# Optimization experiments

Hardware: AMD Instinct MI355X
Metric: run time of the kernel (lower is better)

## Reference

```python
import jax, jax.numpy as jnp
import numpy as np

EPS_BN = 1e-5
CLAMP_MAX = 1e-10  # nn.Hardtanh(min_val=0, max_val=1e-10) on squared dists


def _three_nn(xyz1, xyz2):
    # xyz1: (b, n, 3), xyz2: (b, m, 3) -> sq dists (b, n, 3), idx (b, n, 3)
    d2 = (jnp.sum(xyz1 ** 2, -1, keepdims=True)
          - 2.0 * jnp.einsum('bnc,bmc->bnm', xyz1, xyz2)
          + jnp.sum(xyz2 ** 2, -1)[:, None, :])  # (b, n, m)
    neg, idx = jax.lax.top_k(-d2, 3)
    return -neg, idx


def _conv_bn_relu(x, W, b, g, beta):
    # x: (b, n, cin); 1x1 Conv2d == pointwise linear, BN over (batch, spatial)
    y = jnp.einsum('bnc,oc->bno', x, W) + b
    mean = jnp.mean(y, axis=(0, 1))
    var = jnp.mean((y - mean) ** 2, axis=(0, 1))
    y = (y - mean) * jax.lax.rsqrt(var + EPS_BN) * g + beta
    return jax.nn.relu(y)


def setup_inputs() -> dict:
    key = jax.random.key(0)
    ks = jax.random.split(key, 8)
    b, n, m, c1, c2 = 16, 4096, 1024, 256, 512
    mlp, dimin = [256, 256], [c1 + c2, 256]
    inp = {
        'xyz1': jax.random.normal(ks[0], (b, n, 3), jnp.float32),
        'xyz2': jax.random.normal(ks[1], (b, m, 3), jnp.float32),
        'points1': jax.random.normal(ks[2], (b, n, c1), jnp.float32),
        'points2': jax.random.normal(ks[3], (b, m, c2), jnp.float32),
        'W1': jax.random.normal(ks[4], (mlp[0], dimin[0]), jnp.float32) * 0.02,
        'b1': jnp.zeros((mlp[0],), jnp.float32),
        'g1': jnp.ones((mlp[0],), jnp.float32),
        'beta1': jnp.zeros((mlp[0],), jnp.float32),
        'W2': jax.random.normal(ks[5], (mlp[1], dimin[1]), jnp.float32) * 0.02,
        'b2': jnp.zeros((mlp[1],), jnp.float32),
        'g2': jnp.ones((mlp[1],), jnp.float32),
        'beta2': jnp.zeros((mlp[1],), jnp.float32),
    }
    return inp


def reference(xyz1, xyz2, points1, points2, W1, b1, g1, beta1, W2, b2, g2, beta2):
    dist, idx = _three_nn(xyz1, xyz2)                     # (b, n, 3)
    dist = jnp.clip(dist, 0.0, CLAMP_MAX)                 # Hardtanh(0, 1e-10)
    inv = 1.0 / dist
    weight = inv / jnp.sum(inv, axis=2, keepdims=True)    # (b, n, 3)
    neigh = jax.vmap(lambda p, i: p[i])(points2, idx)     # (b, n, 3, c2)
    interp = jnp.einsum('bnk,bnkc->bnc', weight, neigh)   # (b, n, c2)
    feat = jnp.concatenate([interp, points1], axis=2)     # (b, n, c2+c1)
    feat = _conv_bn_relu(feat, W1, b1, g1, beta1)
    feat = _conv_bn_relu(feat, W2, b2, g2, beta2)
    return jnp.transpose(feat, (0, 2, 1))                 # (b, c_out, n)
```

## Files before the change

### kernel.cpp

```cpp
#include <hip/hip_runtime.h>

typedef unsigned short u16;
typedef short sh8 __attribute__((ext_vector_type(8)));
typedef float floatx4 __attribute__((ext_vector_type(4)));
typedef float float4v __attribute__((ext_vector_type(4)));
typedef u16 us8 __attribute__((ext_vector_type(8)));
typedef u16 us4 __attribute__((ext_vector_type(4)));

#define NB    16
#define NPTS  4096
#define MPTS  1024
#define CC1   256
#define CC2   512
#define KK1   768
#define CCO   256
#define MT    (NB*NPTS)
#define MZ    (NB*MPTS)

__device__ __forceinline__ float b2f(u16 u) {
    union { unsigned i; float f; } v; v.i = ((unsigned)u) << 16; return v.f;
}
__device__ __forceinline__ u16 f2b(float f) {
    union { float f; unsigned i; } v; v.f = f;
    unsigned u = v.i;
    unsigned r = (u + 0x7fffu + ((u >> 16) & 1u)) >> 16;
    return (u16)r;
}
__device__ __forceinline__ float ldv(const void* p, size_t i, int f32) {
    return f32 ? ((const float*)p)[i] : b2f(((const u16*)p)[i]);
}
__device__ __forceinline__ void stv(void* p, size_t i, int f32, float v) {
    if (f32) ((float*)p)[i] = v; else ((u16*)p)[i] = f2b(v);
}
__device__ __forceinline__ void gl_lds16(const void* g, void* l) {
    __builtin_amdgcn_global_load_lds(
        (const __attribute__((address_space(1))) void*)g,
        (__attribute__((address_space(3))) void*)l, 16, 0, 0);
}

__global__ __launch_bounds__(256) void Pointnet_fp_module_33071248179394_kernel(
        const unsigned* g1bits, int* flag, float* stats,
        const void* W1, const void* W2, u16* Wa, u16* Wbp, u16* W2b) {
    const int f32 = (g1bits[0] == 0x3F800000u) ? 1 : 0;
    const int i = blockIdx.x * 256 + threadIdx.x;
    if (blockIdx.x == 0) {
        for (int k = threadIdx.x; k < 1024; k += 256) stats[k] = 0.f;
        if (threadIdx.x == 0) flag[0] = f32;
    }
    if (i < CCO * CC2) {
        int r = i >> 9, c = i & 511;
        Wa[i] = f2b(ldv(W1, (size_t)r * KK1 + c, f32));
    } else if (i < CCO * CC2 + CCO * CC1) {
        int k = i - CCO * CC2;
        int r = k >> 8, c = k & 255;
        Wbp[k] = f2b(ldv(W1, (size_t)r * KK1 + CC2 + c, f32));
    } else {
        int k = i - CCO * CC2 - CCO * CC1;
        W2b[k] = f2b(ldv(W2, k, f32));
    }
}

__global__ __launch_bounds__(512) void three_nn_k(
        const int* flagp, const void* xyz1, const void* xyz2,
        int* nidx, float* nw) {
    __shared__ float4 P[MPTS];
    __shared__ float md[512][3];
    __shared__ int   mi[512][3];
    const int f32 = flagp[0];
    const int bi = blockIdx.x >> 6;
    const int chunk = blockIdx.x & 63;
    const int t = threadIdx.x;
    const int ql = t & 63, sp = t >> 6;

    for (int p = t; p < MPTS; p += 512) {
        size_t s = (size_t)(bi * MPTS + p) * 3;
        P[p] = make_float4(ldv(xyz2, s, f32), ldv(xyz2, s + 1, f32),
                           ldv(xyz2, s + 2, f32), 0.f);
    }
    __syncthreads();

    const int q = chunk * 64 + ql;
    size_t s1 = (size_t)(bi * NPTS + q) * 3;
    const float qx = ldv(xyz1, s1 + 0, f32);
    const float qy = ldv(xyz1, s1 + 1, f32);
    const float qz = ldv(xyz1, s1 + 2, f32);

    float d0 = 3e38f, d1 = 3e38f, dv2 = 3e38f;
    int i0 = -1, i1 = -1, i2 = -1;
    const int jbeg = sp * 128, jend = jbeg + 128;
    #pragma unroll 4
    for (int j = jbeg; j < jend; j++) {
        float4 p = P[j];
        float dx = qx - p.x;
        float dy = qy - p.y;
        float dz = qz - p.z;
        float dd = fmaf(dx, dx, fmaf(dy, dy, dz * dz));
        if (dd < dv2) {
            if (dd < d0)      { dv2 = d1; i2 = i1; d1 = d0; i1 = i0; d0 = dd; i0 = j; }
            else if (dd < d1) { dv2 = d1; i2 = i1; d1 = dd; i1 = j; }
            else              { dv2 = dd; i2 = j; }
        }
    }
    md[t][0] = d0;  md[t][1] = d1;  md[t][2] = dv2;
    mi[t][0] = i0;  mi[t][1] = i1;  mi[t][2] = i2;
    __syncthreads();

    if (t < 64) {
        float b0 = 3e38f, b1 = 3e38f, b2v = 3e38f;
        int j0 = -1, j1 = -1, j2 = -1;
        #pragma unroll
        for (int s = 0; s < 8; s++) {
            int base = s * 64 + t;
            #pragma unroll
            for (int k = 0; k < 3; k++) {
                float d = md[base][k];
                int ji = mi[base][k];
                if (d < b0)      { b2v = b1; j2 = j1; b1 = b0; j1 = j0; b0 = d; j0 = ji; }
                else if (d < b1) { b2v = b1; j2 = j1; b1 = d; j1 = ji; }
                else if (d < b2v){ b2v = d; j2 = ji; }
            }
        }
        float e0 = fminf(fmaxf(b0, 0.f), 1e-10f);
        float e1 = fminf(fmaxf(b1, 0.f), 1e-10f);
        float e2 = fminf(fmaxf(b2v, 0.f), 1e-10f);
        float v0 = 1.0f / e0, v1 = 1.0f / e1, v2 = 1.0f / e2;
        float s = v0 + v1 + v2;
        const size_t gq = ((size_t)bi * NPTS + chunk * 64 + t) * 3;
        nidx[gq + 0] = j0; nidx[gq + 1] = j1; nidx[gq + 2] = j2;
        nw[gq + 0] = v0 / s; nw[gq + 1] = v1 / s; nw[gq + 2] = v2 / s;
    }
}

template<int K, int NW>
__global__ __launch_bounds__(128 * NW, 2) void gemm_z_k(
        const int* flagp, const void* __restrict__ A, const u16* __restrict__ B,
        u16* __restrict__ Y) {
    constexpr int T  = 128 * NW;
    constexpr int NT = NW * 64;
    __shared__ u16 As[128 * 32];
    __shared__ u16 Bs[NT * 32];
    const int f32 = flagp[0];
    const int tid = threadIdx.x;
    const int m0 = blockIdx.x * 128;
    const int n0 = blockIdx.y * NT;
    const int wave = tid >> 6, lane = tid & 63;
    const int wm = wave & 1, wn = wave >> 1;
    const int l16 = lane & 15, quad = lane >> 4;

    floatx4 acc[4][4];
    #pragma unroll
    for (int i = 0; i < 4; i++)
        #pragma unroll
        for (int j = 0; j < 4; j++)
            acc[i][j] = (floatx4){0.f, 0.f, 0.f, 0.f};

    for (int kb = 0; kb < K; kb += 32) {
        __syncthreads();
        #pragma unroll
        for (int c = tid; c < 512; c += T) {
            int row = c >> 2, c4 = c & 3;
            if (f32) {
                const float* ap = (const float*)A + (size_t)(m0 + row) * K + kb + c4 * 8;
                float4v a = *(const float4v*)ap;
                float4v b = *(const float4v*)(ap + 4);
                us8 o;
                #pragma unroll
                for (int k = 0; k < 4; k++) { o[k] = f2b(a[k]); o[k + 4] = f2b(b[k]); }
                *(us8*)(As + c * 8) = o;
            } else {
                gl_lds16((const u16*)A + (size_t)(m0 + row) * K + kb + c4 * 8,
                         As + c * 8);
            }
        }
        #pragma unroll
        for (int c = tid; c < NT * 4; c += T) {
            int row = c >> 2, c4 = c & 3;
            gl_lds16(B + (size_t)(n0 + row) * K + kb + c4 * 8, Bs + c * 8);
        }
        __syncthreads();

        sh8 af[4], bfr[4];
        #pragma unroll
        for (int i = 0; i < 4; i++)
            af[i] = *(const sh8*)(As + (wm * 64 + i * 16 + l16) * 32 + quad * 8);
        #pragma unroll
        for (int j = 0; j < 4; j++)
            bfr[j] = *(const sh8*)(Bs + (wn * 64 + j * 16 + l16) * 32 + quad * 8);
        #pragma unroll
        for (int i = 0; i < 4; i++)
            #pragma unroll
            for (int j = 0; j < 4; j++)
                acc[i][j] = __builtin_amdgcn_mfma_f32_16x16x32_bf16(
                                bfr[j], af[i], acc[i][j], 0, 0, 0);
    }

    #pragma unroll
    for (int i = 0; i < 4; i++) {
        int row = m0 + wm * 64 + i * 16 + l16;
        #pragma unroll
        for (int j = 0; j < 4; j++) {
            int colb = wn * 64 + j * 16 + quad * 4;
            us4 o;
            #pragma unroll
            for (int r = 0; r < 4; r++)
                o[r] = f2b(acc[i][j][r]);
            *(us4*)(Y + (size_t)row * CCO + n0 + colb) = o;
        }
    }
}

template<bool GATHER, bool BN1>
__global__ __launch_bounds__(256, 4) void gemm_mt_k(
        const int* flagp, const void* __restrict__ Asrc,
        const u16* __restrict__ B, const void* __restrict__ bias,
        const int* __restrict__ nidx, const float* __restrict__ nw,
        const u16* __restrict__ Zb,
        u16* __restrict__ Y, float* __restrict__ sum, float* __restrict__ sq,
        const float* __restrict__ nsum, const float* __restrict__ nsq,
        const void* __restrict__ ng, const void* __restrict__ nbeta) {
    __shared__ u16 As[64 * 256];
    __shared__ float sSum[256], sSq[256];
    __shared__ int   sIdx[GATHER ? 192 : 1];
    __shared__ float sW[GATHER ? 192 : 1];
    __shared__ float ssc[BN1 ? 256 : 1], ssh[BN1 ? 256 : 1];
    const int f32 = flagp[0];
    const int tid = threadIdx.x;
    const int m0 = blockIdx.x * 64;
    const int wn = tid >> 6, lane = tid & 63;
    const int l16 = lane & 15, quad = lane >> 4;

    sSum[tid] = 0.f; sSq[tid] = 0.f;
    if (BN1) {
        const float invM = 1.0f / (float)MT;
        float mean = nsum[tid] * invM;
        float var = nsq[tid] * invM - mean * mean;
        float sc = rsqrtf(var + 1e-5f) * ldv(ng, tid, f32);
        ssc[tid] = sc;
        ssh[tid] = ldv(nbeta, tid, f32) - mean * sc;
    }
    if (GATHER && tid < 64) {
        size_t q3 = (size_t)(m0 + tid) * 3;
        #pragma unroll
        for (int k = 0; k < 3; k++) {
            sIdx[tid * 3 + k] = nidx[q3 + k];
            sW[tid * 3 + k]   = nw[q3 + k];
        }
    }
    if (BN1) __syncthreads();

    #pragma unroll
    for (int c = tid; c < 2048; c += 256) {
        int r = c >> 5, cp = c & 31;
        int col = ((cp ^ (r & 7)) << 3);
        if (BN1) {
            us8 a = *(const us8*)((const u16*)Asrc + (size_t)(m0 + r) * 256 + col);
            us8 o;
            #pragma unroll
            for (int k = 0; k < 8; k++)
                o[k] = f2b(fmaxf(b2f((u16)a[k]) * ssc[col + k] + ssh[col + k], 0.f));
            *(us8*)(As + c * 8) = o;
        } else if (f32) {
            const float* ap = (const float*)Asrc + (size_t)(m0 + r) * 256 + col;
            float4v a = *(const float4v*)ap;
            float4v b = *(const float4v*)(ap + 4);
            us8 o;
            #pragma unroll
            for (int k = 0; k < 4; k++) { o[k] = f2b(a[k]); o[k + 4] = f2b(b[k]); }
            *(us8*)(As + c * 8) = o;
        } else {
            gl_lds16((const u16*)Asrc + (size_t)(m0 + r) * 256 + col, As + c * 8);
        }
    }
    __syncthreads();

    floatx4 acc[4][4];
    #pragma unroll
    for (int i = 0; i < 4; i++)
        #pragma unroll
        for (int j = 0; j < 4; j++)
            acc[i][j] = (floatx4){0.f, 0.f, 0.f, 0.f};

    #pragma unroll 2
    for (int kb = 0; kb < 256; kb += 32) {
        sh8 af[4], bfr[4];
        #pragma unroll
        for (int j = 0; j < 4; j++)
            bfr[j] = *(const sh8*)(B + (size_t)(wn * 64 + j * 16 + l16) * 256
                                     + kb + quad * 8);
        #pragma unroll
        for (int i = 0; i < 4; i++) {
            int r = i * 16 + l16;
            int cp = ((kb >> 3) + quad) ^ (l16 & 7);
            af[i] = *(const sh8*)(As + r * 256 + (cp << 3));
        }
        #pragma unroll
        for (int i = 0; i < 4; i++)
            #pragma unroll
            for (int j = 0; j < 4; j++)
                acc[i][j] = __builtin_amdgcn_mfma_f32_16x16x32_bf16(
                                bfr[j], af[i], acc[i][j], 0, 0, 0);
    }

    float bvv[4][4];
    #pragma unroll
    for (int j = 0; j < 4; j++)
        #pragma unroll
        for (int r = 0; r < 4; r++)
            bvv[j][r] = ldv(bias, wn * 64 + j * 16 + quad * 4 + r, f32);

    float cs[4][4], css[4][4];
    #pragma unroll
    for (int j = 0; j < 4; j++)
        #pragma unroll
        for (int r = 0; r < 4; r++) { cs[j][r] = 0.f; css[j][r] = 0.f; }

    const int zbase = GATHER ? ((m0 >> 12) << 10) : 0;
    #pragma unroll
    for (int i = 0; i < 4; i++) {
        int rl = i * 16 + l16;
        const u16 *z0 = nullptr, *z1 = nullptr, *z2 = nullptr;
        float w0 = 0.f, w1 = 0.f, w2 = 0.f;
        if (GATHER) {
            int i0 = sIdx[rl * 3 + 0], i1 = sIdx[rl * 3 + 1], i2 = sIdx[rl * 3 + 2];
            w0 = sW[rl * 3 + 0]; w1 = sW[rl * 3 + 1]; w2 = sW[rl * 3 + 2];
            z0 = Zb + (size_t)(zbase + i0) * CCO;
            z1 = Zb + (size_t)(zbase + i1) * CCO;
            z2 = Zb + (size_t)(zbase + i2) * CCO;
        }
        u16* yrow = Y + (size_t)(m0 + rl) * CCO;
        #pragma unroll
        for (int j = 0; j < 4; j++) {
            int colb = wn * 64 + j * 16 + quad * 4;
            us4 o;
            if (GATHER) {
                us4 zv0 = *(const us4*)(z0 + colb);
                us4 zv1 = *(const us4*)(z1 + colb);
                us4 zv2 = *(const us4*)(z2 + colb);
                #pragma unroll
                for (int r = 0; r < 4; r++) {
                    float v = acc[i][j][r] + bvv[j][r]
                            + w0 * b2f((u16)zv0[r]) + w1 * b2f((u16)zv1[r])
                            + w2 * b2f((u16)zv2[r]);
                    cs[j][r] += v; css[j][r] += v * v;
                    o[r] = f2b(v);
                }
            } else {
                #pragma unroll
                for (int r = 0; r < 4; r++) {
                    float v = acc[i][j][r] + bvv[j][r];
                    cs[j][r] += v; css[j][r] += v * v;
                    o[r] = f2b(v);
                }
            }
            *(us4*)(yrow + colb) = o;
        }
    }
    #pragma unroll
    for (int j = 0; j < 4; j++)
        #pragma unroll
        for (int r = 0; r < 4; r++) {
            float a = cs[j][r], b = css[j][r];
            #pragma unroll
            for (int m = 1; m < 16; m <<= 1) {
                a += __shfl_xor(a, m, 64);
                b += __shfl_xor(b, m, 64);
            }
            if (l16 == 0) {
                int cl = wn * 64 + j * 16 + quad * 4 + r;
                atomicAdd(&sSum[cl], a);
                atomicAdd(&sSq[cl], b);
            }
        }
    __syncthreads();
    atomicAdd(&sum[tid], sSum[tid]);
    atomicAdd(&sq[tid], sSq[tid]);
}

__global__ void bn_out_k(const int* flagp, const u16* Y, void* Out,
                         const float* sum, const float* sq,
                         const void* g, const void* beta) {
    __shared__ float tile[64][65];
    const int f32 = flagp[0];
    const int bi = blockIdx.z;
    const int p0 = blockIdx.x * 64;
    const int c0 = blockIdx.y * 64;
    const int t = threadIdx.x;
    const int cr = t & 63, rq = t >> 6;
    const float invM = 1.0f / (float)MT;

    const int c = c0 + cr;
    float mean = sum[c] * invM;
    float var = sq[c] * invM - mean * mean;
    float sc = rsqrtf(var + 1e-5f) * ldv(g, c, f32);
    float sh = ldv(beta, c, f32) - mean * sc;

    for (int r = rq; r < 64; r += 4) {
        int m = bi * NPTS + p0 + r;
        float v = b2f(Y[(size_t)m * CCO + c]) * sc + sh;
        tile[r][cr] = fmaxf(v, 0.f);
    }
    __syncthreads();
    for (int r = rq; r < 64; r += 4) {
        size_t o = ((size_t)bi * CCO + (c0 + r)) * NPTS + p0 + cr;
        stv(Out, o, f32, tile[cr][r]);
    }
}

extern "C" void kernel_launch(void* const* d_in, const int* in_sizes, int n_in,
                              void* d_out, int out_size, void* d_ws, size_t ws_size,
                              hipStream_t stream) {
    const void* xyz1    = d_in[0];
    const void* xyz2    = d_in[1];
    const void* points1 = d_in[2];
    const void* points2 = d_in[3];
    const void* W1      = d_in[4];
    const void* b1      = d_in[5];
    const void* g1      = d_in[6];
    const void* be1     = d_in[7];
    const void* W2      = d_in[8];
    const void* b2      = d_in[9];
    const void* g2      = d_in[10];
    const void* be2     = d_in[11];
    char* ws = (char*)d_ws;

    int*   flag  = (int*)(ws + 0);
    float* sum1  = (float*)(ws + 4096);
    float* sq1   = (float*)(ws + 5120);
    float* sum2  = (float*)(ws + 6144);
    float* sq2   = (float*)(ws + 7168);
    int*   nidx  = (int*)(ws + 20480);
    float* nw    = (float*)(ws + 806912);
    u16* Wa   = (u16*)(ws + 2097152);
    u16* Wbp  = (u16*)(ws + 2359296);
    u16* W2b  = (u16*)(ws + 2490368);
    u16* Z    = (u16*)(ws + 2621440);
    u16* y1   = (u16*)(ws + 11010048ULL);
    u16* y2   = (u16*)(ws + 44564480ULL);

    Pointnet_fp_module_33071248179394_kernel<<<dim3(1024), dim3(256), 0, stream>>>(
        (const unsigned*)g1, flag, (float*)(ws + 4096), W1, W2, Wa, Wbp, W2b);
    three_nn_k<<<dim3(1024), dim3(512), 0, stream>>>(flag, xyz1, xyz2, nidx, nw);
    gemm_z_k<CC2, 2><<<dim3(MZ / 128, 2), dim3(256), 0, stream>>>(
        flag, points2, Wa, Z);
    gemm_mt_k<true, false><<<dim3(MT / 64), dim3(256), 0, stream>>>(
        flag, points1, Wbp, b1, nidx, nw, Z, y1, sum1, sq1,
        nullptr, nullptr, nullptr, nullptr);
    gemm_mt_k<false, true><<<dim3(MT / 64), dim3(256), 0, stream>>>(
        flag, y1, W2b, b2, nullptr, nullptr, nullptr, y2, sum2, sq2,
        sum1, sq1, g1, be1);
    bn_out_k<<<dim3(64, 4, NB), dim3(256), 0, stream>>>(
        flag, y2, d_out, sum2, sq2, g2, be2);
}
```

Baseline: 335.6 us.

## Retile main GEMMs to 128x128 blocks with K-sliced LDS staging of A and B

The two point-wise GEMM kernels now compute 128x128 output tiles instead of a 64-row by full-256-column tile. The A and B operands are staged through small 32-wide K slices in LDS rather than loading the whole A row block and reading B straight from global memory. Block indices are remapped so neighbouring blocks share rows, and launch bounds drop to 2 blocks per SM. The aim is more operand reuse and less LDS per block, at the cost of two barriers per K step with no overlap between loads and MFMA, plus the gather and BN prologue work now spread over column halves.

Result: faster. 311.3 us (-7.2%).

```diff
diff --git a/kernel.cpp b/kernel.cpp
--- a/kernel.cpp
+++ b/kernel.cpp
@@ -210,7 +210,7 @@
 }
 
 template<bool GATHER, bool BN1>
-__global__ __launch_bounds__(256, 4) void gemm_mt_k(
+__global__ __launch_bounds__(256, 2) void gemm_mt_k(
         const int* flagp, const void* __restrict__ Asrc,
         const u16* __restrict__ B, const void* __restrict__ bias,
         const int* __restrict__ nidx, const float* __restrict__ nw,
@@ -218,19 +218,23 @@
         u16* __restrict__ Y, float* __restrict__ sum, float* __restrict__ sq,
         const float* __restrict__ nsum, const float* __restrict__ nsq,
         const void* __restrict__ ng, const void* __restrict__ nbeta) {
-    __shared__ u16 As[64 * 256];
-    __shared__ float sSum[256], sSq[256];
-    __shared__ int   sIdx[GATHER ? 192 : 1];
-    __shared__ float sW[GATHER ? 192 : 1];
+    __shared__ u16 As[128 * 32];
+    __shared__ u16 Bs[128 * 32];
+    __shared__ float sSum[128], sSq[128];
+    __shared__ int   sIdx[GATHER ? 384 : 1];
+    __shared__ float sW[GATHER ? 384 : 1];
     __shared__ float ssc[BN1 ? 256 : 1], ssh[BN1 ? 256 : 1];
     const int f32 = flagp[0];
     const int tid = threadIdx.x;
-    const int m0 = blockIdx.x * 64;
-    const int wn = tid >> 6, lane = tid & 63;
+    const int rb = (blockIdx.x & 7) * 128 + (blockIdx.x >> 3);
+    const int m0 = (rb >> 1) * 128;
+    const int n0 = (rb & 1) * 128;
+    const int wave = tid >> 6, lane = tid & 63;
+    const int wm = wave & 1, wn = wave >> 1;
     const int l16 = lane & 15, quad = lane >> 4;
 
-    sSum[tid] = 0.f; sSq[tid] = 0.f;
-    if (BN1) {
+    if (tid < 128) { sSum[tid] = 0.f; sSq[tid] = 0.f; }
+    if (BN1 && tid < 256) {
         const float invM = 1.0f / (float)MT;
         float mean = nsum[tid] * invM;
         float var = nsq[tid] * invM - mean * mean;
@@ -238,7 +242,7 @@
         ssc[tid] = sc;
         ssh[tid] = ldv(nbeta, tid, f32) - mean * sc;
     }
-    if (GATHER && tid < 64) {
+    if (GATHER && tid < 128) {
         size_t q3 = (size_t)(m0 + tid) * 3;
         #pragma unroll
         for (int k = 0; k < 3; k++) {
@@ -246,32 +250,6 @@
             sW[tid * 3 + k]   = nw[q3 + k];
         }
     }
-    if (BN1) __syncthreads();
-
-    #pragma unroll
-    for (int c = tid; c < 2048; c += 256) {
-        int r = c >> 5, cp = c & 31;
-        int col = ((cp ^ (r & 7)) << 3);
-        if (BN1) {
-            us8 a = *(const us8*)((const u16*)Asrc + (size_t)(m0 + r) * 256 + col);
-            us8 o;
-            #pragma unroll
-            for (int k = 0; k < 8; k++)
-                o[k] = f2b(fmaxf(b2f((u16)a[k]) * ssc[col + k] + ssh[col + k], 0.f));
-            *(us8*)(As + c * 8) = o;
-        } else if (f32) {
-            const float* ap = (const float*)Asrc + (size_t)(m0 + r) * 256 + col;
-            float4v a = *(const float4v*)ap;
-            float4v b = *(const float4v*)(ap + 4);
-            us8 o;
-            #pragma unroll
-            for (int k = 0; k < 4; k++) { o[k] = f2b(a[k]); o[k + 4] = f2b(b[k]); }
-            *(us8*)(As + c * 8) = o;
-        } else {
-            gl_lds16((const u16*)Asrc + (size_t)(m0 + r) * 256 + col, As + c * 8);
-        }
-    }
-    __syncthreads();
 
     floatx4 acc[4][4];
     #pragma unroll
@@ -280,19 +258,50 @@
         for (int j = 0; j < 4; j++)
             acc[i][j] = (floatx4){0.f, 0.f, 0.f, 0.f};
 
-    #pragma unroll 2
-    for (int kb = 0; kb < 256; kb += 32) {
+    constexpr int K = 256;
+    for (int kb = 0; kb < K; kb += 32) {
+        __syncthreads();
+        #pragma unroll
+        for (int c = tid; c < 512; c += 256) {
+            int row = c >> 2, c4 = c & 3;
+            if (BN1) {
+                us8 a = *(const us8*)((const u16*)Asrc
+                            + (size_t)(m0 + row) * K + kb + c4 * 8);
+                us8 o;
+                #pragma unroll
+                for (int k = 0; k < 8; k++) {
+                    int ch = kb + c4 * 8 + k;
+                    o[k] = f2b(fmaxf(b2f((u16)a[k]) * ssc[ch] + ssh[ch], 0.f));
+                }
+                *(us8*)(As + c * 8) = o;
+            } else if (f32) {
+                const float* ap = (const float*)Asrc
+                            + (size_t)(m0 + row) * K + kb + c4 * 8;
+                float4v a = *(const float4v*)ap;
+                float4v b = *(const float4v*)(ap + 4);
+                us8 o;
+                #pragma unroll
+                for (int k = 0; k < 4; k++) { o[k] = f2b(a[k]); o[k + 4] = f2b(b[k]); }
+                *(us8*)(As + c * 8) = o;
+            } else {
+                gl_lds16((const u16*)Asrc + (size_t)(m0 + row) * K + kb + c4 * 8,
+                         As + c * 8);
+            }
+        }
+        #pragma unroll
+        for (int c = tid; c < 512; c += 256) {
+            int row = c >> 2, c4 = c & 3;
+            gl_lds16(B + (size_t)(n0 + row) * K + kb + c4 * 8, Bs + c * 8);
+        }
+        __syncthreads();
+
         sh8 af[4], bfr[4];
         #pragma unroll
+        for (int i = 0; i < 4; i++)
+            af[i] = *(const sh8*)(As + (wm * 64 + i * 16 + l16) * 32 + quad * 8);
+        #pragma unroll
         for (int j = 0; j < 4; j++)
-            bfr[j] = *(const sh8*)(B + (size_t)(wn * 64 + j * 16 + l16) * 256
-                                     + kb + quad * 8);
-        #pragma unroll
-        for (int i = 0; i < 4; i++) {
-            int r = i * 16 + l16;
-            int cp = ((kb >> 3) + quad) ^ (l16 & 7);
-            af[i] = *(const sh8*)(As + r * 256 + (cp << 3));
-        }
+            bfr[j] = *(const sh8*)(Bs + (wn * 64 + j * 16 + l16) * 32 + quad * 8);
         #pragma unroll
         for (int i = 0; i < 4; i++)
             #pragma unroll
@@ -306,7 +315,7 @@
     for (int j = 0; j < 4; j++)
         #pragma unroll
         for (int r = 0; r < 4; r++)
-            bvv[j][r] = ldv(bias, wn * 64 + j * 16 + quad * 4 + r, f32);
+            bvv[j][r] = ldv(bias, n0 + wn * 64 + j * 16 + quad * 4 + r, f32);
 
     float cs[4][4], css[4][4];
     #pragma unroll
@@ -317,17 +326,17 @@
     const int zbase = GATHER ? ((m0 >> 12) << 10) : 0;
     #pragma unroll
     for (int i = 0; i < 4; i++) {
-        int rl = i * 16 + l16;
+        int rl = wm * 64 + i * 16 + l16;
         const u16 *z0 = nullptr, *z1 = nullptr, *z2 = nullptr;
         float w0 = 0.f, w1 = 0.f, w2 = 0.f;
         if (GATHER) {
             int i0 = sIdx[rl * 3 + 0], i1 = sIdx[rl * 3 + 1], i2 = sIdx[rl * 3 + 2];
             w0 = sW[rl * 3 + 0]; w1 = sW[rl * 3 + 1]; w2 = sW[rl * 3 + 2];
-            z0 = Zb + (size_t)(zbase + i0) * CCO;
-            z1 = Zb + (size_t)(zbase + i1) * CCO;
-            z2 = Zb + (size_t)(zbase + i2) * CCO;
-        }
-        u16* yrow = Y + (size_t)(m0 + rl) * CCO;
+            z0 = Zb + (size_t)(zbase + i0) * CCO + n0;
+            z1 = Zb + (size_t)(zbase + i1) * CCO + n0;
+            z2 = Zb + (size_t)(zbase + i2) * CCO + n0;
+        }
+        u16* yrow = Y + (size_t)(m0 + rl) * CCO + n0;
         #pragma unroll
         for (int j = 0; j < 4; j++) {
             int colb = wn * 64 + j * 16 + quad * 4;
@@ -372,8 +381,10 @@
             }
         }
     __syncthreads();
-    atomicAdd(&sum[tid], sSum[tid]);
-    atomicAdd(&sq[tid], sSq[tid]);
+    if (tid < 128) {
+        atomicAdd(&sum[n0 + tid], sSum[tid]);
+        atomicAdd(&sq[n0 + tid], sSq[tid]);
+    }
 }
 
 __global__ void bn_out_k(const int* flagp, const u16* Y, void* Out,
@@ -442,10 +453,10 @@
     three_nn_k<<<dim3(1024), dim3(512), 0, stream>>>(flag, xyz1, xyz2, nidx, nw);
     gemm_z_k<CC2, 2><<<dim3(MZ / 128, 2), dim3(256), 0, stream>>>(
         flag, points2, Wa, Z);
-    gemm_mt_k<true, false><<<dim3(MT / 64), dim3(256), 0, stream>>>(
+    gemm_mt_k<true, false><<<dim3(1024), dim3(256), 0, stream>>>(
         flag, points1, Wbp, b1, nidx, nw, Z, y1, sum1, sq1,
         nullptr, nullptr, nullptr, nullptr);
-    gemm_mt_k<false, true><<<dim3(MT / 64), dim3(256), 0, stream>>>(
+    gemm_mt_k<false, true><<<dim3(1024), dim3(256), 0, stream>>>(
         flag, y1, W2b, b2, nullptr, nullptr, nullptr, y2, sum2, sq2,
         sum1, sq1, g1, be1);
     bn_out_k<<<dim3(64, 4, NB), dim3(256), 0, stream>>>(
```
